# Performance work log

Measured on AMD Instinct MI355X. Metric: run time of the kernel, lower is better.

Reference implementation:

```python
import jax, jax.numpy as jnp
import numpy as np

B = 2097152
NUM_CLASSES = 8
CANCER_IDX = jnp.array([0, 1, 3], dtype=jnp.int32)
FN_MULT = 3.0
MEL_FN_MULT = 5.0
RECALL_W = 0.5
TEMP = 1.5
HARD_MINING = True
CANCER_SMOOTH = 0.05
BENIGN_SMOOTH = 0.1
HARD_WEIGHT = 2.0


def setup_inputs() -> dict:
    key = jax.random.key(0)
    k1, k2, k3 = jax.random.split(key, 3)
    logits = jax.random.normal(k1, (B, NUM_CLASSES), dtype=jnp.float32)
    targets = jax.random.randint(k2, (B,), 0, NUM_CLASSES, dtype=jnp.int32)
    class_counts = jax.random.uniform(k3, (NUM_CLASSES,), dtype=jnp.float32,
                                      minval=100.0, maxval=10000.0)
    return {"logits": logits, "targets": targets, "class_counts": class_counts}


def reference(logits, targets, class_counts):
    C = NUM_CLASSES
    dt = logits.dtype
    cancer_mask = jnp.zeros((C,), dtype=dt).at[CANCER_IDX].set(1.0)  # [C]
    n_cancer = CANCER_IDX.shape[0]

    # class weights: 1/sqrt(count+1), normalized to sum to C
    w = 1.0 / jnp.sqrt(class_counts + 1.0)
    base_weight = w / w.sum() * C

    # asymmetric label smoothing (vectorized)
    is_cancer_t = cancer_mask[targets] > 0  # [B] bool
    smooth = jnp.where(is_cancer_t, CANCER_SMOOTH, BENIGN_SMOOTH).astype(dt)  # [B]
    onehot = jax.nn.one_hot(targets, C, dtype=dt)  # [B, C]
    smoothed = smooth[:, None] / C + onehot * (1.0 - smooth)[:, None]
    # benign samples with smooth>0: redistribute extra mass onto cancer classes
    extra = jnp.where((~is_cancer_t) & (smooth > 0), smooth * 0.5 / n_cancer, 0.0)
    smoothed = smoothed + extra[:, None] * cancer_mask[None, :]
    smoothed = smoothed / smoothed.sum(axis=1, keepdims=True)  # no-op for rows summing to 1

    # temperature-scaled weighted CE
    log_probs = jax.nn.log_softmax(logits / TEMP, axis=1)
    ce = -(smoothed * log_probs).sum(axis=1)  # [B]
    ce = ce * base_weight[targets]

    # FN multipliers from hard argmax predictions
    preds = jnp.argmax(logits, axis=1)
    is_cancer_p = cancer_mask[preds] > 0
    mult = jnp.where(is_cancer_t & (~is_cancer_p), FN_MULT, 1.0)
    mult = jnp.where((targets == 0) & (~is_cancer_p), MEL_FN_MULT, mult)
    ce = ce * mult.astype(dt)

    if HARD_MINING:
        hard = is_cancer_t & (preds != targets)
        ce = ce * jnp.where(hard, HARD_WEIGHT, 1.0).astype(dt)

    base_loss = ce.mean()

    # soft recall loss over cancer-class probability mass
    probs = jax.nn.softmax(logits, axis=1)
    cancer_probs = probs @ cancer_mask  # [B]
    isc = is_cancer_t.astype(dt)
    soft_tp = (cancer_probs * isc).sum()
    soft_fn = ((1.0 - cancer_probs) * isc).sum()
    soft_recall = soft_tp / (soft_tp + soft_fn + 1e-8)
    recall_loss = 1.0 - soft_recall

    return base_loss + RECALL_W * recall_loss
```

## Files before the change

kernel.cpp:

```cpp
#include <hip/hip_runtime.h>


constexpr int C   = 8;
constexpr int NT  = 512;
constexpr int NB  = 1024;
constexpr int RPT = 4;

__device__ __forceinline__ float wave_reduce_sum(float v) {
    #pragma unroll
    for (int off = 32; off > 0; off >>= 1) v += __shfl_down(v, off, 64);
    return v;
}

__device__ __forceinline__ void row_loss(const float l[8], int t, float bw,
                                         float& ce_sum, float& tp_sum,
                                         float& cnt_sum) {
    const float inv_temp = 1.0f / 1.5f;
    const float c_uni   = 0.05f / 8.0f;
    const float c_one   = 1.0f - 0.05f;
    const float b_uni   = 0.1f / 8.0f;
    const float b_one   = 1.0f - 0.1f;
    const float b_extra = 0.1f * 0.5f / 3.0f;
    const float b_norm  = 1.0f / (1.0f + 3.0f * (0.1f * 0.5f / 3.0f));

    float m = l[0];
    int   p = 0;
    #pragma unroll
    for (int j = 1; j < 8; ++j) { if (l[j] > m) { m = l[j]; p = j; } }

    float se = 0.0f, e0, e1, e3;
    {
        float e[8];
        #pragma unroll
        for (int j = 0; j < 8; ++j) { e[j] = __expf(l[j] - m); se += e[j]; }
        e0 = e[0]; e1 = e[1]; e3 = e[3];
    }
    const float cp = (e0 + e1 + e3) / se;

    float se2 = 0.0f;
    #pragma unroll
    for (int j = 0; j < 8; ++j) se2 += __expf((l[j] - m) * inv_temp);
    const float logZ = m * inv_temp + __logf(se2);

    float S = 0.0f;
    #pragma unroll
    for (int j = 0; j < 8; ++j) S += l[j];
    const float X  = S * inv_temp;
    const float Xc = (l[0] + l[1] + l[3]) * inv_temp;
    float lt = l[0];
    #pragma unroll
    for (int j = 1; j < 8; ++j) lt = (t == j) ? l[j] : lt;
    const float xt = lt * inv_temp;

    const bool isct = ((1u << t) & 0xBu) != 0u;
    const bool iscp = ((1u << p) & 0xBu) != 0u;

    float dot;
    if (isct) dot = c_uni * X + c_one * xt;
    else      dot = (b_uni * X + b_one * xt + b_extra * Xc) * b_norm;

    float ce = (logZ - dot) * bw;

    float mult = (isct && !iscp) ? 3.0f : 1.0f;
    if (t == 0 && !iscp) mult = 5.0f;
    if (isct && p != t) mult *= 2.0f;
    ce *= mult;

    ce_sum += ce;
    if (isct) { tp_sum += cp; cnt_sum += 1.0f; }
}

__global__ __launch_bounds__(NT) void mrl_pass1(
    const float* __restrict__ logits,
    const int*   __restrict__ targets,
    const float* __restrict__ counts,
    float*       __restrict__ part,
    int B)
{
    __shared__ float s_red[(NT / 64) * 3];

    float w[C];
    float ws = 0.0f;
    #pragma unroll
    for (int c = 0; c < C; ++c) { w[c] = rsqrtf(counts[c] + 1.0f); ws += w[c]; }
    const float scale = (float)C / ws;

    float ce_sum = 0.0f, tp_sum = 0.0f, cnt_sum = 0.0f;

    const long tid  = (long)blockIdx.x * NT + threadIdx.x;
    const long base = tid * RPT;

    if (base + RPT <= B) {
        const float4* rowp = reinterpret_cast<const float4*>(logits + base * 8);
        float4 r[2 * RPT];
        #pragma unroll
        for (int q = 0; q < 2 * RPT; ++q) r[q] = rowp[q];
        const int4 t4 = *reinterpret_cast<const int4*>(targets + base);
        const int ts[RPT] = {t4.x, t4.y, t4.z, t4.w};

        #pragma unroll
        for (int j = 0; j < RPT; ++j) {
            const int t = ts[j];
            float bw = w[0];
            #pragma unroll
            for (int c = 1; c < C; ++c) bw = (t == c) ? w[c] : bw;
            bw *= scale;
            const float l[8] = {r[2*j].x,   r[2*j].y,   r[2*j].z,   r[2*j].w,
                                r[2*j+1].x, r[2*j+1].y, r[2*j+1].z, r[2*j+1].w};
            row_loss(l, t, bw, ce_sum, tp_sum, cnt_sum);
        }
    } else {
        for (long i = base; i < B; ++i) {
            const float4* row = reinterpret_cast<const float4*>(logits + i * 8);
            const float4 a = row[0];
            const float4 b = row[1];
            const float l[8] = {a.x, a.y, a.z, a.w, b.x, b.y, b.z, b.w};
            const int t = targets[i];
            float bw = w[0];
            #pragma unroll
            for (int c = 1; c < C; ++c) bw = (t == c) ? w[c] : bw;
            bw *= scale;
            row_loss(l, t, bw, ce_sum, tp_sum, cnt_sum);
        }
    }

    float v0 = wave_reduce_sum(ce_sum);
    float v1 = wave_reduce_sum(tp_sum);
    float v2 = wave_reduce_sum(cnt_sum);
    const int lane = threadIdx.x & 63;
    const int wid  = threadIdx.x >> 6;
    if (lane == 0) {
        s_red[wid * 3 + 0] = v0;
        s_red[wid * 3 + 1] = v1;
        s_red[wid * 3 + 2] = v2;
    }
    __syncthreads();
    if (threadIdx.x == 0) {
        float r0 = 0.0f, r1 = 0.0f, r2 = 0.0f;
        #pragma unroll
        for (int w2 = 0; w2 < NT / 64; ++w2) {
            r0 += s_red[w2 * 3 + 0];
            r1 += s_red[w2 * 3 + 1];
            r2 += s_red[w2 * 3 + 2];
        }
        part[blockIdx.x]          = r0;
        part[NB + blockIdx.x]     = r1;
        part[2 * NB + blockIdx.x] = r2;
    }
}

__global__ __launch_bounds__(64) void mrl_pass2(
    const float* __restrict__ part,
    float*       __restrict__ out,
    int B)
{
    const float4* p4 = reinterpret_cast<const float4*>(part);
    const int lane = threadIdx.x;
    constexpr int SEG = NB / 4;

    float4 a[4], b[4], c[4];
    #pragma unroll
    for (int q = 0; q < 4; ++q) a[q] = p4[lane + q * 64];
    #pragma unroll
    for (int q = 0; q < 4; ++q) b[q] = p4[SEG + lane + q * 64];
    #pragma unroll
    for (int q = 0; q < 4; ++q) c[q] = p4[2 * SEG + lane + q * 64];

    float ce = 0.0f, tp = 0.0f, cnt = 0.0f;
    #pragma unroll
    for (int q = 0; q < 4; ++q) {
        ce  += (a[q].x + a[q].y) + (a[q].z + a[q].w);
        tp  += (b[q].x + b[q].y) + (b[q].z + b[q].w);
        cnt += (c[q].x + c[q].y) + (c[q].z + c[q].w);
    }
    ce  = wave_reduce_sum(ce);
    tp  = wave_reduce_sum(tp);
    cnt = wave_reduce_sum(cnt);
    if (lane == 0) {
        const float base_loss   = ce / (float)B;
        const float recall_loss = 1.0f - tp / (cnt + 1e-8f);
        out[0] = base_loss + 0.5f * recall_loss;
    }
}

extern "C" void kernel_launch(void* const* d_in, const int* in_sizes, int n_in,
                              void* d_out, int out_size, void* d_ws, size_t ws_size,
                              hipStream_t stream) {
    const float* logits  = (const float*)d_in[0];
    const int*   targets = (const int*)d_in[1];
    const float* counts  = (const float*)d_in[2];
    float* out  = (float*)d_out;
    float* part = (float*)d_ws;
    const int B = in_sizes[1];

    mrl_pass1<<<NB, NT, 0, stream>>>(logits, targets, counts, part, B);
    mrl_pass2<<<1, 64, 0, stream>>>(part, out, B);
}
```

Measured before the change: 23.72 us.

## Fuse two-pass reduction into one kernel with atomic counter handoff

Merges the per-block partial reduction and the final reduction into a single launch. A dedicated last block spins on striped atomic counters until every worker block has published its partials, then reduces them and writes the loss. Block size and grid change to 2047 workers of 256 threads using a grid-stride loop. A memset is added to reset the counters each call, and the approach relies on the reducer block not starving the workers.

```diff
diff --git a/kernel.cpp b/kernel.cpp
--- a/kernel.cpp
+++ b/kernel.cpp
@@ -1,14 +1,19 @@
 #include <hip/hip_runtime.h>
 
 
-constexpr int C   = 8;
-constexpr int NT  = 512;
-constexpr int NB  = 1024;
-constexpr int RPT = 4;
-
-__device__ __forceinline__ float wave_reduce_sum(float v) {
-    #pragma unroll
-    for (int off = 32; off > 0; off >>= 1) v += __shfl_down(v, off, 64);
+constexpr int C    = 8;
+constexpr int NT   = 256;
+constexpr int NBW  = 2047;
+constexpr int NCTR = 64;
+
+__device__ __forceinline__ float wave_bfly_sum(float v) {
+    #pragma unroll
+    for (int off = 1; off < 64; off <<= 1) v += __shfl_xor(v, off, 64);
+    return v;
+}
+__device__ __forceinline__ unsigned wave_bfly_sum_u(unsigned v) {
+    #pragma unroll
+    for (int off = 1; off < 64; off <<= 1) v += __shfl_xor(v, off, 64);
     return v;
 }
 
@@ -70,116 +75,116 @@
     if (isct) { tp_sum += cp; cnt_sum += 1.0f; }
 }
 
-__global__ __launch_bounds__(NT) void mrl_pass1(
+__global__ __launch_bounds__(NT) void mrl_fused(
     const float* __restrict__ logits,
     const int*   __restrict__ targets,
     const float* __restrict__ counts,
-    float*       __restrict__ part,
+    float*        part,
+    unsigned int* ctr,
+    float*        out,
     int B)
 {
     __shared__ float s_red[(NT / 64) * 3];
-
-    float w[C];
-    float ws = 0.0f;
-    #pragma unroll
-    for (int c = 0; c < C; ++c) { w[c] = rsqrtf(counts[c] + 1.0f); ws += w[c]; }
-    const float scale = (float)C / ws;
-
-    float ce_sum = 0.0f, tp_sum = 0.0f, cnt_sum = 0.0f;
-
-    const long tid  = (long)blockIdx.x * NT + threadIdx.x;
-    const long base = tid * RPT;
-
-    if (base + RPT <= B) {
-        const float4* rowp = reinterpret_cast<const float4*>(logits + base * 8);
-        float4 r[2 * RPT];
-        #pragma unroll
-        for (int q = 0; q < 2 * RPT; ++q) r[q] = rowp[q];
-        const int4 t4 = *reinterpret_cast<const int4*>(targets + base);
-        const int ts[RPT] = {t4.x, t4.y, t4.z, t4.w};
-
-        #pragma unroll
-        for (int j = 0; j < RPT; ++j) {
-            const int t = ts[j];
-            float bw = w[0];
-            #pragma unroll
-            for (int c = 1; c < C; ++c) bw = (t == c) ? w[c] : bw;
-            bw *= scale;
-            const float l[8] = {r[2*j].x,   r[2*j].y,   r[2*j].z,   r[2*j].w,
-                                r[2*j+1].x, r[2*j+1].y, r[2*j+1].z, r[2*j+1].w};
-            row_loss(l, t, bw, ce_sum, tp_sum, cnt_sum);
-        }
-    } else {
-        for (long i = base; i < B; ++i) {
-            const float4* row = reinterpret_cast<const float4*>(logits + i * 8);
-            const float4 a = row[0];
-            const float4 b = row[1];
-            const float l[8] = {a.x, a.y, a.z, a.w, b.x, b.y, b.z, b.w};
-            const int t = targets[i];
-            float bw = w[0];
-            #pragma unroll
-            for (int c = 1; c < C; ++c) bw = (t == c) ? w[c] : bw;
-            bw *= scale;
-            row_loss(l, t, bw, ce_sum, tp_sum, cnt_sum);
-        }
-    }
-
-    float v0 = wave_reduce_sum(ce_sum);
-    float v1 = wave_reduce_sum(tp_sum);
-    float v2 = wave_reduce_sum(cnt_sum);
+    const int bid  = blockIdx.x;
     const int lane = threadIdx.x & 63;
     const int wid  = threadIdx.x >> 6;
-    if (lane == 0) {
-        s_red[wid * 3 + 0] = v0;
-        s_red[wid * 3 + 1] = v1;
-        s_red[wid * 3 + 2] = v2;
-    }
-    __syncthreads();
-    if (threadIdx.x == 0) {
-        float r0 = 0.0f, r1 = 0.0f, r2 = 0.0f;
+
+    if (bid != NBW) {
+        float w[C];
+        float ws = 0.0f;
         #pragma unroll
-        for (int w2 = 0; w2 < NT / 64; ++w2) {
-            r0 += s_red[w2 * 3 + 0];
-            r1 += s_red[w2 * 3 + 1];
-            r2 += s_red[w2 * 3 + 2];
-        }
-        part[blockIdx.x]          = r0;
-        part[NB + blockIdx.x]     = r1;
-        part[2 * NB + blockIdx.x] = r2;
-    }
-}
-
-__global__ __launch_bounds__(64) void mrl_pass2(
-    const float* __restrict__ part,
-    float*       __restrict__ out,
-    int B)
-{
-    const float4* p4 = reinterpret_cast<const float4*>(part);
-    const int lane = threadIdx.x;
-    constexpr int SEG = NB / 4;
-
-    float4 a[4], b[4], c[4];
-    #pragma unroll
-    for (int q = 0; q < 4; ++q) a[q] = p4[lane + q * 64];
-    #pragma unroll
-    for (int q = 0; q < 4; ++q) b[q] = p4[SEG + lane + q * 64];
-    #pragma unroll
-    for (int q = 0; q < 4; ++q) c[q] = p4[2 * SEG + lane + q * 64];
-
-    float ce = 0.0f, tp = 0.0f, cnt = 0.0f;
-    #pragma unroll
-    for (int q = 0; q < 4; ++q) {
-        ce  += (a[q].x + a[q].y) + (a[q].z + a[q].w);
-        tp  += (b[q].x + b[q].y) + (b[q].z + b[q].w);
-        cnt += (c[q].x + c[q].y) + (c[q].z + c[q].w);
-    }
-    ce  = wave_reduce_sum(ce);
-    tp  = wave_reduce_sum(tp);
-    cnt = wave_reduce_sum(cnt);
-    if (lane == 0) {
-        const float base_loss   = ce / (float)B;
-        const float recall_loss = 1.0f - tp / (cnt + 1e-8f);
-        out[0] = base_loss + 0.5f * recall_loss;
+        for (int c = 0; c < C; ++c) { w[c] = rsqrtf(counts[c] + 1.0f); ws += w[c]; }
+        const float scale = (float)C / ws;
+
+        float ce_sum = 0.0f, tp_sum = 0.0f, cnt_sum = 0.0f;
+
+        const int NQ   = B >> 2;
+        const int nthr = NBW * NT;
+        for (int q = bid * NT + threadIdx.x; q < NQ; q += nthr) {
+            const long base = (long)q * 4;
+            const float4* rowp = reinterpret_cast<const float4*>(logits + base * 8);
+            float4 r[8];
+            #pragma unroll
+            for (int k = 0; k < 8; ++k) r[k] = rowp[k];
+            const int4 t4 = *reinterpret_cast<const int4*>(targets + base);
+            const int ts[4] = {t4.x, t4.y, t4.z, t4.w};
+
+            #pragma unroll
+            for (int j = 0; j < 4; ++j) {
+                const int t = ts[j];
+                float bw = w[0];
+                #pragma unroll
+                for (int c = 1; c < C; ++c) bw = (t == c) ? w[c] : bw;
+                bw *= scale;
+                const float l[8] = {r[2*j].x,   r[2*j].y,   r[2*j].z,   r[2*j].w,
+                                    r[2*j+1].x, r[2*j+1].y, r[2*j+1].z, r[2*j+1].w};
+                row_loss(l, t, bw, ce_sum, tp_sum, cnt_sum);
+            }
+        }
+
+        float v0 = wave_bfly_sum(ce_sum);
+        float v1 = wave_bfly_sum(tp_sum);
+        float v2 = wave_bfly_sum(cnt_sum);
+        if (lane == 0) {
+            s_red[wid * 3 + 0] = v0;
+            s_red[wid * 3 + 1] = v1;
+            s_red[wid * 3 + 2] = v2;
+        }
+        __syncthreads();
+        if (threadIdx.x == 0) {
+            float r0 = 0.0f, r1 = 0.0f, r2 = 0.0f;
+            #pragma unroll
+            for (int w2 = 0; w2 < NT / 64; ++w2) {
+                r0 += s_red[w2 * 3 + 0];
+                r1 += s_red[w2 * 3 + 1];
+                r2 += s_red[w2 * 3 + 2];
+            }
+            __hip_atomic_store(&part[bid],           r0, __ATOMIC_RELAXED, __HIP_MEMORY_SCOPE_AGENT);
+            __hip_atomic_store(&part[NBW + bid],     r1, __ATOMIC_RELAXED, __HIP_MEMORY_SCOPE_AGENT);
+            __hip_atomic_store(&part[2 * NBW + bid], r2, __ATOMIC_RELAXED, __HIP_MEMORY_SCOPE_AGENT);
+            asm volatile("s_waitcnt vmcnt(0)" ::: "memory");
+            __hip_atomic_fetch_add(&ctr[bid & (NCTR - 1)], 1u,
+                                   __ATOMIC_RELAXED, __HIP_MEMORY_SCOPE_AGENT);
+        }
+    } else {
+        if (wid == 0) {
+            for (;;) {
+                unsigned v = (lane < NCTR)
+                    ? __hip_atomic_load(&ctr[lane], __ATOMIC_RELAXED, __HIP_MEMORY_SCOPE_AGENT)
+                    : 0u;
+                if (wave_bfly_sum_u(v) == (unsigned)NBW) break;
+                __builtin_amdgcn_s_sleep(8);
+            }
+        }
+        __syncthreads();
+
+        float ce = 0.0f, tp = 0.0f, cnt = 0.0f;
+        for (int k = threadIdx.x; k < NBW; k += NT) {
+            ce  += __hip_atomic_load(&part[k],           __ATOMIC_RELAXED, __HIP_MEMORY_SCOPE_AGENT);
+            tp  += __hip_atomic_load(&part[NBW + k],     __ATOMIC_RELAXED, __HIP_MEMORY_SCOPE_AGENT);
+            cnt += __hip_atomic_load(&part[2 * NBW + k], __ATOMIC_RELAXED, __HIP_MEMORY_SCOPE_AGENT);
+        }
+        float v0 = wave_bfly_sum(ce);
+        float v1 = wave_bfly_sum(tp);
+        float v2 = wave_bfly_sum(cnt);
+        if (lane == 0) {
+            s_red[wid * 3 + 0] = v0;
+            s_red[wid * 3 + 1] = v1;
+            s_red[wid * 3 + 2] = v2;
+        }
+        __syncthreads();
+        if (threadIdx.x == 0) {
+            float r0 = 0.0f, r1 = 0.0f, r2 = 0.0f;
+            #pragma unroll
+            for (int w2 = 0; w2 < NT / 64; ++w2) {
+                r0 += s_red[w2 * 3 + 0];
+                r1 += s_red[w2 * 3 + 1];
+                r2 += s_red[w2 * 3 + 2];
+            }
+            const float base_loss   = r0 / (float)B;
+            const float recall_loss = 1.0f - r1 / (r2 + 1e-8f);
+            out[0] = base_loss + 0.5f * recall_loss;
+        }
     }
 }
 
@@ -191,8 +196,10 @@
     const float* counts  = (const float*)d_in[2];
     float* out  = (float*)d_out;
     float* part = (float*)d_ws;
+    unsigned int* ctr = (unsigned int*)((char*)d_ws + 24576);
+
     const int B = in_sizes[1];
 
-    mrl_pass1<<<NB, NT, 0, stream>>>(logits, targets, counts, part, B);
-    mrl_pass2<<<1, 64, 0, stream>>>(part, out, B);
-}
+    hipMemsetAsync(ctr, 0, NCTR * sizeof(unsigned int), stream);
+    mrl_fused<<<NBW + 1, NT, 0, stream>>>(logits, targets, counts, part, ctr, out, B);
+}
```

Result: slower. 33.43 us (+40.9%).
